# Kernel tuning notes

Measured on AMD Instinct MI355X. Metric: run time of the kernel, lower is better.

Reference implementation:

```python
import jax, jax.numpy as jnp
import numpy as np

B, T, D = 4, 1024, 1024
H, S = 16, 64            # n_heads, stalk_dim
HID = 3072               # int(D*3.0), already even
P_ADIC_BASE, P_ADIC_MAX = 2, 16


def quant6(w):
    # per-tensor symmetric 6-bit fake-quant (abs-max scale, round, clamp)
    scale = jnp.abs(w).max() / 31.0 + 1e-8
    return jnp.clip(jnp.round(w / scale), -31, 31) * scale


def q6_ste(w):
    # straight-through estimator: identity gradient
    return w + jax.lax.stop_gradient(quant6(w) - w)


def layernorm(x, g, b, eps=1e-5):
    mu = x.mean(-1, keepdims=True)
    var = ((x - mu) ** 2).mean(-1, keepdims=True)
    return (x - mu) * jax.lax.rsqrt(var + eps) * g + b


def build_p_adic_bias(t, p=P_ADIC_BASE, max_val=P_ADIC_MAX):
    idx = np.arange(t)
    d = np.abs(idx[:, None] - idx[None, :])
    nz = d > 0
    vp = np.zeros_like(d)
    work = d.copy()
    while True:
        div = nz & (work % p == 0)
        if not div.any():
            break
        vp = vp + div.astype(vp.dtype)
        work = np.where(div, work // p, work)
    vals = np.minimum(vp, max_val).astype(np.float32)
    vals = np.where(nz, vals, np.float32(max_val))
    return jnp.asarray(vals / max_val)


def setup_inputs() -> dict:
    key = jax.random.key(0)
    ks = jax.random.split(key, 12)
    sd_d = 1.0 / np.sqrt(D)
    sd_s = 1.0 / np.sqrt(S)
    sd_h = 1.0 / np.sqrt(HID)
    return {
        "x": jax.random.normal(ks[0], (B, T, D), jnp.float32),
        "wq": jax.random.normal(ks[1], (D, D), jnp.float32) * sd_d,
        "wk": jax.random.normal(ks[2], (D, D), jnp.float32) * sd_d,
        "wv": jax.random.normal(ks[3], (D, D), jnp.float32) * sd_d,
        "wo": jax.random.normal(ks[4], (D, D), jnp.float32) * sd_d,
        "su": jax.random.normal(ks[5], (S, S), jnp.float32) * sd_s,
        "sv": jax.random.normal(ks[6], (S, S), jnp.float32) * sd_s,
        "p_scale": jnp.ones((1,), jnp.float32) * 0.1,
        "norm1_g": jnp.ones((D,), jnp.float32),
        "norm1_b": jnp.zeros((D,), jnp.float32),
        "norm2_g": jnp.ones((D,), jnp.float32),
        "norm2_b": jnp.zeros((D,), jnp.float32),
        "w_up": jax.random.normal(ks[7], (HID, D), jnp.float32) * sd_d,
        "w_down": jax.random.normal(ks[8], (D, HID), jnp.float32) * sd_h,
        "theta": jnp.zeros((HID // 2,), jnp.float32),
        "mlp_norm_g": jnp.ones((HID,), jnp.float32),
        "mlp_norm_b": jnp.zeros((HID,), jnp.float32),
    }


def _sheaf_attention(xn, wq, wk, wv, wo, su, sv, p_scale):
    # projections with inline 6-bit fake-quant of weights
    Q = (xn @ q6_ste(wq).T).reshape(B, T, H, S).transpose(0, 2, 1, 3)  # [B,H,T,S]
    K = (xn @ q6_ste(wk).T).reshape(B, T, H, S).transpose(0, 2, 1, 3)
    V = (xn @ q6_ste(wv).T).reshape(B, T, H, S).transpose(0, 2, 1, 3)
    Qs = Q @ q6_ste(su).T   # stalk map on head dim
    Ks = K @ q6_ste(sv).T
    scale = 1.0 / np.sqrt(S)
    scores = jnp.einsum('bhts,bhus->bhtu', Qs, Ks) * scale
    p_bias = build_p_adic_bias(T)                     # [T,T], constant
    scores = scores + p_scale[0] * p_bias[None, None]
    causal = jnp.triu(jnp.ones((T, T), bool), k=1)
    scores = jnp.where(causal[None, None], -jnp.inf, scores)
    attn = jax.nn.softmax(scores, axis=-1)
    out = jnp.einsum('bhtu,bhus->bhts', attn, V)
    out = out.transpose(0, 2, 1, 3).reshape(B, T, D)
    return out @ q6_ste(wo).T


def _so2_mlp(xn, w_up, w_down, theta, ng, nb):
    h = xn @ q6_ste(w_up).T                          # [B,T,HID]
    hp = h.reshape(B, T, HID // 2, 2)
    a, b = hp[..., 0], hp[..., 1]
    c, s = jnp.cos(theta), jnp.sin(theta)            # [HID/2]
    rot = jnp.stack([c * a - s * b, s * a + c * b], axis=-1).reshape(B, T, HID)
    rot = layernorm(rot, ng, nb)
    rot = jax.nn.silu(rot)
    return rot @ q6_ste(w_down).T


def reference(x, wq, wk, wv, wo, su, sv, p_scale, norm1_g, norm1_b,
              norm2_g, norm2_b, w_up, w_down, theta, mlp_norm_g, mlp_norm_b):
    # pre-norm residual block: x = x + attn(ln1(x)); x = x + mlp(ln2(x))
    x = x + _sheaf_attention(layernorm(x, norm1_g, norm1_b),
                             wq, wk, wv, wo, su, sv, p_scale)
    x = x + _so2_mlp(layernorm(x, norm2_g, norm2_b),
                     w_up, w_down, theta, mlp_norm_g, mlp_norm_b)
    return x
```

## Files before the change

### kernel.cpp

```cpp
#include <hip/hip_runtime.h>
#include <stdint.h>

typedef __bf16 bf16;
typedef __attribute__((ext_vector_type(8))) __bf16 bf16x8;
typedef __attribute__((ext_vector_type(4))) __bf16 bf16x4;
typedef __attribute__((ext_vector_type(2))) __bf16 bf16x2;
typedef __attribute__((ext_vector_type(4))) float f32x4;

#define GLOBAL_AS __attribute__((address_space(1)))
#define LDS_AS __attribute__((address_space(3)))

static __device__ __forceinline__ bf16 f2bf(float f) {
  unsigned u = __builtin_bit_cast(unsigned, f);
  u += 0x7fffu + ((u >> 16) & 1u);
  unsigned short h = (unsigned short)(u >> 16);
  return __builtin_bit_cast(bf16, h);
}

static __device__ __forceinline__ float waveSum(float v) {
  #pragma unroll
  for (int o = 32; o > 0; o >>= 1) v += __shfl_xor(v, o);
  return v;
}
static __device__ __forceinline__ float waveMax(float v) {
  #pragma unroll
  for (int o = 32; o > 0; o >>= 1) v = fmaxf(v, __shfl_xor(v, o));
  return v;
}

struct QTask { const float* src; bf16* dst; int n; int slot; int blk0; };
struct QTasks { QTask t[8]; };

__global__ __launch_bounds__(256) void absmax_all(QTasks qt, unsigned* amax) {
  int ti = 0;
  #pragma unroll
  for (int i = 1; i < 8; ++i) if ((int)blockIdx.x >= qt.t[i].blk0) ti = i;
  const QTask tk = qt.t[ti];
  const int base = (blockIdx.x - tk.blk0) * 4096;
  const float4* s4 = (const float4*)(tk.src + base);
  float m = 0.f;
  #pragma unroll
  for (int i = 0; i < 4; ++i) {
    float4 w = s4[i * 256 + threadIdx.x];
    m = fmaxf(m, fmaxf(fmaxf(fabsf(w.x), fabsf(w.y)), fmaxf(fabsf(w.z), fabsf(w.w))));
  }
  m = waveMax(m);
  __shared__ float red[4];
  if ((threadIdx.x & 63) == 0) red[threadIdx.x >> 6] = m;
  __syncthreads();
  if (threadIdx.x == 0) {
    float mm = fmaxf(fmaxf(red[0], red[1]), fmaxf(red[2], red[3]));
    atomicMax(amax + tk.slot, __float_as_uint(mm));
  }
}

__global__ __launch_bounds__(256) void quant_all(QTasks qt, const unsigned* amax) {
  int ti = 0;
  #pragma unroll
  for (int i = 1; i < 8; ++i) if ((int)blockIdx.x >= qt.t[i].blk0) ti = i;
  const QTask tk = qt.t[ti];
  const float scale = __uint_as_float(amax[tk.slot]) / 31.0f + 1e-8f;
  const int base = (blockIdx.x - tk.blk0) * 4096;
  const float4* s4 = (const float4*)(tk.src + base);
  bf16x4* d4 = (bf16x4*)(tk.dst + base);
  #pragma unroll
  for (int i = 0; i < 4; ++i) {
    float4 w = s4[i * 256 + threadIdx.x];
    bf16x4 o;
    float q;
    q = fminf(31.f, fmaxf(-31.f, rintf(w.x / scale))); o[0] = f2bf(q * scale);
    q = fminf(31.f, fmaxf(-31.f, rintf(w.y / scale))); o[1] = f2bf(q * scale);
    q = fminf(31.f, fmaxf(-31.f, rintf(w.z / scale))); o[2] = f2bf(q * scale);
    q = fminf(31.f, fmaxf(-31.f, rintf(w.w / scale))); o[3] = f2bf(q * scale);
    d4[i * 256 + threadIdx.x] = o;
  }
}

__global__ __launch_bounds__(256) void ln_kernel(const float* __restrict__ x,
                                                 const float* __restrict__ g,
                                                 const float* __restrict__ b,
                                                 bf16* __restrict__ out) {
  const int row = blockIdx.x, tid = threadIdx.x;
  const float4 v = ((const float4*)(x + (size_t)row * 1024))[tid];
  float s = v.x + v.y + v.z + v.w;
  float ss = v.x * v.x + v.y * v.y + v.z * v.z + v.w * v.w;
  s = waveSum(s); ss = waveSum(ss);
  __shared__ float rs[4], rq[4];
  if ((tid & 63) == 0) { rs[tid >> 6] = s; rq[tid >> 6] = ss; }
  __syncthreads();
  s = rs[0] + rs[1] + rs[2] + rs[3];
  ss = rq[0] + rq[1] + rq[2] + rq[3];
  const float mu = s * (1.f / 1024.f);
  const float var = ss * (1.f / 1024.f) - mu * mu;
  const float rstd = rsqrtf(var + 1e-5f);
  const float4 gv = ((const float4*)g)[tid];
  const float4 bv = ((const float4*)b)[tid];
  bf16x4 o;
  o[0] = f2bf((v.x - mu) * rstd * gv.x + bv.x);
  o[1] = f2bf((v.y - mu) * rstd * gv.y + bv.y);
  o[2] = f2bf((v.z - mu) * rstd * gv.z + bv.z);
  o[3] = f2bf((v.w - mu) * rstd * gv.w + bv.w);
  ((bf16x4*)(out + (size_t)row * 1024))[tid] = o;
}

__global__ __launch_bounds__(256) void gemm_bt(const bf16* __restrict__ A,
                                               const bf16* __restrict__ B,
                                               bf16* __restrict__ C,
                                               int M, int N, int K) {
  constexpr int BM = 128, BN = 128, BK = 32;
  __shared__ bf16 As[BM * BK];
  __shared__ bf16 Bs[BN * BK];
  const int tid = threadIdx.x;
  const int wave = tid >> 6, lane = tid & 63, quad = lane >> 4, l16 = lane & 15;
  const int bm0 = blockIdx.y * BM, bn0 = blockIdx.x * BN;
  const int wr = (wave >> 1) * 64, wc = (wave & 1) * 64;
  f32x4 acc[4][4] = {};

  for (int k0 = 0; k0 < K; k0 += BK) {
    __syncthreads();
    #pragma unroll
    for (int i = 0; i < 2; ++i) {
      const int id = tid + i * 256;
      const int r = id >> 2, c = (id & 3) * 8;
      __builtin_amdgcn_global_load_lds(
          (GLOBAL_AS void*)(A + (size_t)(bm0 + r) * K + k0 + c),
          (LDS_AS void*)(As + (size_t)(i * 256 + wave * 64) * 8), 16, 0, 0);
      __builtin_amdgcn_global_load_lds(
          (GLOBAL_AS void*)(B + (size_t)(bn0 + r) * K + k0 + c),
          (LDS_AS void*)(Bs + (size_t)(i * 256 + wave * 64) * 8), 16, 0, 0);
    }
    __syncthreads();
    bf16x8 af[4], bfr[4];
    #pragma unroll
    for (int mi = 0; mi < 4; ++mi)
      af[mi] = *(const bf16x8*)(As + (wr + mi * 16 + l16) * BK + quad * 8);
    #pragma unroll
    for (int ni = 0; ni < 4; ++ni)
      bfr[ni] = *(const bf16x8*)(Bs + (wc + ni * 16 + l16) * BK + quad * 8);
    #pragma unroll
    for (int mi = 0; mi < 4; ++mi)
      #pragma unroll
      for (int ni = 0; ni < 4; ++ni)
        acc[mi][ni] = __builtin_amdgcn_mfma_f32_16x16x32_bf16(af[mi], bfr[ni], acc[mi][ni], 0, 0, 0);
  }

  #pragma unroll
  for (int mi = 0; mi < 4; ++mi)
    #pragma unroll
    for (int ni = 0; ni < 4; ++ni)
      #pragma unroll
      for (int reg = 0; reg < 4; ++reg) {
        const int row = bm0 + wr + mi * 16 + quad * 4 + reg;
        const int col = bn0 + wc + ni * 16 + l16;
        C[(size_t)row * N + col] = f2bf(acc[mi][ni][reg]);
      }
}

__global__ __launch_bounds__(256) void gemm_bt_split(const bf16* __restrict__ A,
                                                     const bf16* __restrict__ B,
                                                     float* __restrict__ P,
                                                     int M, int N, int Kfull, int Kper) {
  constexpr int BM = 128, BN = 128, BK = 32;
  __shared__ bf16 As[BM * BK];
  __shared__ bf16 Bs[BN * BK];
  const int tid = threadIdx.x;
  const int wave = tid >> 6, lane = tid & 63, quad = lane >> 4, l16 = lane & 15;
  const int bm0 = blockIdx.y * BM, bn0 = blockIdx.x * BN;
  const int wr = (wave >> 1) * 64, wc = (wave & 1) * 64;
  const int kbeg = blockIdx.z * Kper, kend = kbeg + Kper;
  float* Pz = P + (size_t)blockIdx.z * M * N;
  f32x4 acc[4][4] = {};

  for (int k0 = kbeg; k0 < kend; k0 += BK) {
    __syncthreads();
    #pragma unroll
    for (int i = 0; i < 2; ++i) {
      const int id = tid + i * 256;
      const int r = id >> 2, c = (id & 3) * 8;
      __builtin_amdgcn_global_load_lds(
          (GLOBAL_AS void*)(A + (size_t)(bm0 + r) * Kfull + k0 + c),
          (LDS_AS void*)(As + (size_t)(i * 256 + wave * 64) * 8), 16, 0, 0);
      __builtin_amdgcn_global_load_lds(
          (GLOBAL_AS void*)(B + (size_t)(bn0 + r) * Kfull + k0 + c),
          (LDS_AS void*)(Bs + (size_t)(i * 256 + wave * 64) * 8), 16, 0, 0);
    }
    __syncthreads();
    bf16x8 af[4], bfr[4];
    #pragma unroll
    for (int mi = 0; mi < 4; ++mi)
      af[mi] = *(const bf16x8*)(As + (wr + mi * 16 + l16) * BK + quad * 8);
    #pragma unroll
    for (int ni = 0; ni < 4; ++ni)
      bfr[ni] = *(const bf16x8*)(Bs + (wc + ni * 16 + l16) * BK + quad * 8);
    #pragma unroll
    for (int mi = 0; mi < 4; ++mi)
      #pragma unroll
      for (int ni = 0; ni < 4; ++ni)
        acc[mi][ni] = __builtin_amdgcn_mfma_f32_16x16x32_bf16(af[mi], bfr[ni], acc[mi][ni], 0, 0, 0);
  }

  #pragma unroll
  for (int mi = 0; mi < 4; ++mi)
    #pragma unroll
    for (int ni = 0; ni < 4; ++ni)
      #pragma unroll
      for (int reg = 0; reg < 4; ++reg) {
        const int row = bm0 + wr + mi * 16 + quad * 4 + reg;
        const int col = bn0 + wc + ni * 16 + l16;
        Pz[(size_t)row * N + col] = acc[mi][ni][reg];
      }
}

__global__ __launch_bounds__(256) void reduce_wo_ln(const float* __restrict__ x,
                                                    const float* __restrict__ P,
                                                    const float* __restrict__ g,
                                                    const float* __restrict__ b,
                                                    float* __restrict__ y,
                                                    bf16* __restrict__ lnout) {
  const int row = blockIdx.x, tid = threadIdx.x;
  const size_t base = (size_t)row * 1024;
  const float4 vx = ((const float4*)(x + base))[tid];
  const float4 p0 = ((const float4*)(P + base))[tid];
  const float4 p1 = ((const float4*)(P + base + (size_t)4096 * 1024))[tid];
  float4 v;
  v.x = vx.x + p0.x + p1.x;
  v.y = vx.y + p0.y + p1.y;
  v.z = vx.z + p0.z + p1.z;
  v.w = vx.w + p0.w + p1.w;
  ((float4*)(y + base))[tid] = v;
  float s = v.x + v.y + v.z + v.w;
  float ss = v.x * v.x + v.y * v.y + v.z * v.z + v.w * v.w;
  s = waveSum(s); ss = waveSum(ss);
  __shared__ float rs[4], rq[4];
  if ((tid & 63) == 0) { rs[tid >> 6] = s; rq[tid >> 6] = ss; }
  __syncthreads();
  s = rs[0] + rs[1] + rs[2] + rs[3];
  ss = rq[0] + rq[1] + rq[2] + rq[3];
  const float mu = s * (1.f / 1024.f);
  const float var = ss * (1.f / 1024.f) - mu * mu;
  const float rstd = rsqrtf(var + 1e-5f);
  const float4 gv = ((const float4*)g)[tid];
  const float4 bv = ((const float4*)b)[tid];
  bf16x4 o;
  o[0] = f2bf((v.x - mu) * rstd * gv.x + bv.x);
  o[1] = f2bf((v.y - mu) * rstd * gv.y + bv.y);
  o[2] = f2bf((v.z - mu) * rstd * gv.z + bv.z);
  o[3] = f2bf((v.w - mu) * rstd * gv.w + bv.w);
  ((bf16x4*)(lnout + base))[tid] = o;
}

__global__ __launch_bounds__(256) void reduce_down(float* __restrict__ y,
                                                   const float* __restrict__ P) {
  const size_t i = (size_t)blockIdx.x * 256 + threadIdx.x;
  const float4 vy = ((const float4*)y)[i];
  const float4 p0 = ((const float4*)P)[i];
  const float4 p1 = ((const float4*)(P + (size_t)4096 * 1024))[i];
  float4 v;
  v.x = vy.x + p0.x + p1.x;
  v.y = vy.y + p0.y + p1.y;
  v.z = vy.z + p0.z + p1.z;
  v.w = vy.w + p0.w + p1.w;
  ((float4*)y)[i] = v;
}

__global__ __launch_bounds__(256) void stalk_kernel(const bf16* __restrict__ QKV,
                                                    const bf16* __restrict__ Su,
                                                    const bf16* __restrict__ Sv,
                                                    bf16* __restrict__ Qsout,
                                                    bf16* __restrict__ Ksout) {
  constexpr int LDP = 72;
  const int sel = blockIdx.y;
  const bf16* W = sel ? Sv : Su;
  const bf16* src = QKV + (sel ? 1024 : 0);
  bf16* out = sel ? Ksout : Qsout;
  const int vbase = blockIdx.x * 128;
  const int tid = threadIdx.x, wave = tid >> 6, lane = tid & 63, quad = lane >> 4, l16 = lane & 15;
  __shared__ bf16 Ws[64 * LDP];
  #pragma unroll
  for (int i = 0; i < 2; ++i) {
    const int cid = tid + i * 256;
    const int n = cid >> 3, c8 = (cid & 7) * 8;
    *(bf16x8*)(Ws + n * LDP + c8) = *(const bf16x8*)(W + n * 64 + c8);
  }
  __syncthreads();
  f32x4 acc[2][4] = {};
  #pragma unroll
  for (int mi = 0; mi < 2; ++mi) {
    const int v = vbase + wave * 32 + mi * 16 + l16;
    const bf16* arow = src + (size_t)(v >> 4) * 3072 + (v & 15) * 64;
    const bf16x8 a0 = *(const bf16x8*)(arow + quad * 8);
    const bf16x8 a1 = *(const bf16x8*)(arow + 32 + quad * 8);
    #pragma unroll
    for (int ni = 0; ni < 4; ++ni) {
      const bf16x8 b0 = *(const bf16x8*)(Ws + (ni * 16 + l16) * LDP + quad * 8);
      const bf16x8 b1 = *(const bf16x8*)(Ws + (ni * 16 + l16) * LDP + 32 + quad * 8);
      acc[mi][ni] = __builtin_amdgcn_mfma_f32_16x16x32_bf16(a0, b0, acc[mi][ni], 0, 0, 0);
      acc[mi][ni] = __builtin_amdgcn_mfma_f32_16x16x32_bf16(a1, b1, acc[mi][ni], 0, 0, 0);
    }
  }
  #pragma unroll
  for (int mi = 0; mi < 2; ++mi)
    #pragma unroll
    for (int ni = 0; ni < 4; ++ni)
      #pragma unroll
      for (int reg = 0; reg < 4; ++reg) {
        const int v = vbase + wave * 32 + mi * 16 + quad * 4 + reg;
        const int b = v >> 14, t = (v >> 4) & 1023, h = v & 15;
        out[(((size_t)(b * 16 + h)) * 1024 + t) * 64 + ni * 16 + l16] = f2bf(acc[mi][ni][reg]);
      }
}

__global__ __launch_bounds__(256) void v_transpose(const bf16* __restrict__ QKV,
                                                   bf16* __restrict__ Vt) {
  constexpr int LDP = 72;
  const int bh = blockIdx.x, b = bh >> 4, h = bh & 15;
  const int t0 = blockIdx.y * 64;
  const int tid = threadIdx.x;
  __shared__ bf16 tile[64 * LDP];
  #pragma unroll
  for (int i = 0; i < 2; ++i) {
    const int cid = tid + i * 256;
    const int t = cid >> 3, c8 = (cid & 7) * 8;
    *(bf16x8*)(tile + t * LDP + c8) =
        *(const bf16x8*)(QKV + ((size_t)(b * 1024 + t0 + t)) * 3072 + 2048 + h * 64 + c8);
  }
  __syncthreads();
  #pragma unroll
  for (int i = 0; i < 2; ++i) {
    const int cid = tid + i * 256;
    const int s = cid >> 3, t8 = (cid & 7) * 8;
    bf16x8 o;
    #pragma unroll
    for (int j = 0; j < 8; ++j) o[j] = tile[(t8 + j) * LDP + s];
    *(bf16x8*)(Vt + ((size_t)(bh * 64 + s)) * 1024 + t0 + t8) = o;
  }
}

__global__ __launch_bounds__(256) void attn_flash(const bf16* __restrict__ Qs,
                                                  const bf16* __restrict__ Ks,
                                                  const bf16* __restrict__ Vtg,
                                                  const float* __restrict__ p_scale_ptr,
                                                  bf16* __restrict__ out) {
  constexpr int LDP = 72;
  const int bh = blockIdx.x;
  const int b = bh >> 4, h = bh & 15;
  const int ttile = 15 - (int)blockIdx.y;
  const int t0 = ttile * 64;
  const int tid = threadIdx.x, wave = tid >> 6, lane = tid & 63, quad = lane >> 4, l16 = lane & 15;

  __shared__ bf16 Kst[64 * LDP];
  __shared__ bf16 Vt[64 * LDP];
  __shared__ bf16 Plds[4][16 * LDP];

  const float pscale2 = p_scale_ptr[0] * 1.44269504f;
  const float sc2 = 0.125f * 1.44269504f;

  const bf16* Qb = Qs + ((size_t)bh * 1024 + t0) * 64;
  const bf16* Kb = Ks + ((size_t)bh * 1024) * 64;
  const bf16* Vb = Vtg + ((size_t)bh * 64) * 1024;

  const int trow = wave * 16 + l16;
  const bf16x8 qf0 = *(const bf16x8*)(Qb + trow * 64 + quad * 8);
  const bf16x8 qf1 = *(const bf16x8*)(Qb + trow * 64 + 32 + quad * 8);

  float m[4], lsum[4];
  f32x4 Oacc[4] = {};
  #pragma unroll
  for (int r = 0; r < 4; ++r) { m[r] = -1e30f; lsum[r] = 0.f; }

  bf16x8 st[4];
  auto loadTile = [&](int u0) {
    #pragma unroll
    for (int i = 0; i < 2; ++i) {
      const int cid = tid + i * 256;
      st[i] = *(const bf16x8*)(Kb + (size_t)u0 * 64 + cid * 8);
      st[2 + i] = *(const bf16x8*)(Vb + (size_t)(cid >> 3) * 1024 + u0 + (cid & 7) * 8);
    }
  };
  loadTile(0);

  for (int ut = 0; ut <= ttile; ++ut) {
    const int u0 = ut * 64;
    #pragma unroll
    for (int i = 0; i < 2; ++i) {
      const int cid = tid + i * 256;
      const int r = cid >> 3, c8 = (cid & 7) * 8;
      *(bf16x8*)(Kst + r * LDP + c8) = st[i];
      *(bf16x8*)(Vt + r * LDP + c8) = st[2 + i];
    }
    __syncthreads();
    if (ut < ttile) loadTile(u0 + 64);

    f32x4 sc[4];
    #pragma unroll
    for (int ni = 0; ni < 4; ++ni) {
      const bf16x8 k0 = *(const bf16x8*)(Kst + (ni * 16 + l16) * LDP + quad * 8);
      const bf16x8 k1 = *(const bf16x8*)(Kst + (ni * 16 + l16) * LDP + 32 + quad * 8);
      f32x4 z = {};
      z = __builtin_amdgcn_mfma_f32_16x16x32_bf16(qf0, k0, z, 0, 0, 0);
      z = __builtin_amdgcn_mfma_f32_16x16x32_bf16(qf1, k1, z, 0, 0, 0);
      sc[ni] = z;
    }
    const bool diag = (ut == ttile);
    float pv[4][4];
    #pragma unroll
    for (int reg = 0; reg < 4; ++reg) {
      const int t = t0 + wave * 16 + quad * 4 + reg;
      float mx = -1e30f;
      #pragma unroll
      for (int ni = 0; ni < 4; ++ni) {
        const int u = u0 + ni * 16 + l16;
        const int d = t - u;
        float v = sc[ni][reg] * sc2;
        if (diag && d < 0) {
          v = -1e30f;
        } else {
          const float bias = (d == 0) ? 1.0f : (float)__builtin_ctz(d) * 0.0625f;
          v += pscale2 * bias;
        }
        pv[reg][ni] = v;
        mx = fmaxf(mx, v);
      }
      #pragma unroll
      for (int o = 1; o < 16; o <<= 1) mx = fmaxf(mx, __shfl_xor(mx, o));
      const float mnew = fmaxf(m[reg], mx);
      const float alpha = exp2f(m[reg] - mnew);
      m[reg] = mnew;
      float rs = 0.f;
      #pragma unroll
      for (int ni = 0; ni < 4; ++ni) {
        const float p = exp2f(pv[reg][ni] - mnew);
        pv[reg][ni] = p;
        rs += p;
      }
      #pragma unroll
      for (int o = 1; o < 16; o <<= 1) rs += __shfl_xor(rs, o);
      lsum[reg] = lsum[reg] * alpha + rs;
      #pragma unroll
      for (int ni = 0; ni < 4; ++ni) Oacc[ni][reg] *= alpha;
    }
    #pragma unroll
    for (int reg = 0; reg < 4; ++reg)
      #pragma unroll
      for (int ni = 0; ni < 4; ++ni)
        Plds[wave][(quad * 4 + reg) * LDP + ni * 16 + l16] = f2bf(pv[reg][ni]);
    const bf16x8 pf0 = *(const bf16x8*)(&Plds[wave][l16 * LDP + quad * 8]);
    const bf16x8 pf1 = *(const bf16x8*)(&Plds[wave][l16 * LDP + 32 + quad * 8]);
    #pragma unroll
    for (int ni = 0; ni < 4; ++ni) {
      const bf16x8 v0 = *(const bf16x8*)(Vt + (ni * 16 + l16) * LDP + quad * 8);
      const bf16x8 v1 = *(const bf16x8*)(Vt + (ni * 16 + l16) * LDP + 32 + quad * 8);
      Oacc[ni] = __builtin_amdgcn_mfma_f32_16x16x32_bf16(pf0, v0, Oacc[ni], 0, 0, 0);
      Oacc[ni] = __builtin_amdgcn_mfma_f32_16x16x32_bf16(pf1, v1, Oacc[ni], 0, 0, 0);
    }
    __syncthreads();
  }

  #pragma unroll
  for (int ni = 0; ni < 4; ++ni)
    #pragma unroll
    for (int reg = 0; reg < 4; ++reg) {
      const int t = t0 + wave * 16 + quad * 4 + reg;
      out[((size_t)(b * 1024 + t)) * 1024 + h * 64 + ni * 16 + l16] = f2bf(Oacc[ni][reg] / lsum[reg]);
    }
}

__global__ __launch_bounds__(256) void rot_ln_silu(const bf16* __restrict__ hb,
                                                   const float* __restrict__ theta,
                                                   const float* __restrict__ g,
                                                   const float* __restrict__ bb,
                                                   bf16* __restrict__ out) {
  const int row = blockIdx.x, tid = threadIdx.x;
  const bf16* hr = hb + (size_t)row * 3072;
  float r[12];
  float s = 0.f, ss = 0.f;
  #pragma unroll
  for (int i = 0; i < 6; ++i) {
    const int p = tid + i * 256;
    const bf16x2 ab = *(const bf16x2*)(hr + 2 * p);
    const float a = (float)ab[0], b_ = (float)ab[1];
    const float th = theta[p];
    const float c = cosf(th), sn = sinf(th);
    const float r0 = c * a - sn * b_;
    const float r1 = sn * a + c * b_;
    r[2 * i] = r0; r[2 * i + 1] = r1;
    s += r0 + r1;
    ss += r0 * r0 + r1 * r1;
  }
  s = waveSum(s); ss = waveSum(ss);
  __shared__ float rs_[4], rq_[4];
  if ((tid & 63) == 0) { rs_[tid >> 6] = s; rq_[tid >> 6] = ss; }
  __syncthreads();
  s = rs_[0] + rs_[1] + rs_[2] + rs_[3];
  ss = rq_[0] + rq_[1] + rq_[2] + rq_[3];
  const float mu = s * (1.f / 3072.f);
  const float var = ss * (1.f / 3072.f) - mu * mu;
  const float rstd = rsqrtf(var + 1e-5f);
  bf16* orow = out + (size_t)row * 3072;
  #pragma unroll
  for (int i = 0; i < 6; ++i) {
    const int p = tid + i * 256;
    const float2 gv = *(const float2*)(g + 2 * p);
    const float2 bv = *(const float2*)(bb + 2 * p);
    const float y0 = (r[2 * i] - mu) * rstd * gv.x + bv.x;
    const float y1 = (r[2 * i + 1] - mu) * rstd * gv.y + bv.y;
    const float o0 = y0 / (1.f + expf(-y0));
    const float o1 = y1 / (1.f + expf(-y1));
    bf16x2 o; o[0] = f2bf(o0); o[1] = f2bf(o1);
    *(bf16x2*)(orow + 2 * p) = o;
  }
}

extern "C" void kernel_launch(void* const* d_in, const int* in_sizes, int n_in,
                              void* d_out, int out_size, void* d_ws, size_t ws_size,
                              hipStream_t stream) {
  const float* x    = (const float*)d_in[0];
  const float* wq   = (const float*)d_in[1];
  const float* wk   = (const float*)d_in[2];
  const float* wv   = (const float*)d_in[3];
  const float* wo   = (const float*)d_in[4];
  const float* su   = (const float*)d_in[5];
  const float* sv   = (const float*)d_in[6];
  const float* psc  = (const float*)d_in[7];
  const float* n1g  = (const float*)d_in[8];
  const float* n1b  = (const float*)d_in[9];
  const float* n2g  = (const float*)d_in[10];
  const float* n2b  = (const float*)d_in[11];
  const float* wup  = (const float*)d_in[12];
  const float* wdn  = (const float*)d_in[13];
  const float* th   = (const float*)d_in[14];
  const float* mg   = (const float*)d_in[15];
  const float* mb   = (const float*)d_in[16];
  float* outp = (float*)d_out;

  char* ws = (char*)d_ws;
  size_t off = 0;
  auto alloc = [&](size_t bytes) { size_t o = off; off += (bytes + 255) & ~(size_t)255; return o; };
  unsigned* amax = (unsigned*)(ws + alloc(32));
  bf16* Wqkv  = (bf16*)(ws + alloc((size_t)3072 * 1024 * 2));
  bf16* Wo    = (bf16*)(ws + alloc((size_t)1024 * 1024 * 2));
  bf16* Su    = (bf16*)(ws + alloc((size_t)64 * 64 * 2));
  bf16* Sv    = (bf16*)(ws + alloc((size_t)64 * 64 * 2));
  bf16* Wup   = (bf16*)(ws + alloc((size_t)3072 * 1024 * 2));
  bf16* Wdn   = (bf16*)(ws + alloc((size_t)1024 * 3072 * 2));
  bf16* lnbuf = (bf16*)(ws + alloc((size_t)4096 * 1024 * 2));
  bf16* QKVb  = (bf16*)(ws + alloc((size_t)4096 * 3072 * 2));
  bf16* Qsb   = (bf16*)(ws + alloc((size_t)65536 * 64 * 2));
  bf16* Ksb   = (bf16*)(ws + alloc((size_t)65536 * 64 * 2));
  bf16* Vtg   = (bf16*)(ws + alloc((size_t)64 * 64 * 1024 * 2));
  bf16* attno = (bf16*)(ws + alloc((size_t)4096 * 1024 * 2));
  float* Pbuf = (float*)(ws + alloc((size_t)2 * 4096 * 1024 * 4));
  bf16* hbuf = QKVb;
  bf16* gbuf = Qsb;

  hipMemsetAsync(amax, 0, 32, stream);

  QTasks qt;
  int blk = 0;
  auto add = [&](int i, const float* s, bf16* d, int n) {
    qt.t[i].src = s; qt.t[i].dst = d; qt.t[i].n = n; qt.t[i].slot = i; qt.t[i].blk0 = blk;
    blk += n / 4096;
  };
  add(0, wq, Wqkv, 1024 * 1024);
  add(1, wk, Wqkv + (size_t)1024 * 1024, 1024 * 1024);
  add(2, wv, Wqkv + (size_t)2048 * 1024, 1024 * 1024);
  add(3, wo, Wo, 1024 * 1024);
  add(4, su, Su, 4096);
  add(5, sv, Sv, 4096);
  add(6, wup, Wup, 3072 * 1024);
  add(7, wdn, Wdn, 3072 * 1024);

  absmax_all<<<blk, 256, 0, stream>>>(qt, amax);
  quant_all<<<blk, 256, 0, stream>>>(qt, amax);

  ln_kernel<<<4096, 256, 0, stream>>>(x, n1g, n1b, lnbuf);
  gemm_bt<<<dim3(24, 32), 256, 0, stream>>>(lnbuf, Wqkv, QKVb, 4096, 3072, 1024);
  stalk_kernel<<<dim3(512, 2), 256, 0, stream>>>(QKVb, Su, Sv, Qsb, Ksb);
  v_transpose<<<dim3(64, 16), 256, 0, stream>>>(QKVb, Vtg);
  attn_flash<<<dim3(64, 16), 256, 0, stream>>>(Qsb, Ksb, Vtg, psc, attno);
  gemm_bt_split<<<dim3(8, 32, 2), 256, 0, stream>>>(attno, Wo, Pbuf, 4096, 1024, 1024, 512);
  reduce_wo_ln<<<4096, 256, 0, stream>>>(x, Pbuf, n2g, n2b, outp, lnbuf);
  gemm_bt<<<dim3(24, 32), 256, 0, stream>>>(lnbuf, Wup, hbuf, 4096, 3072, 1024);
  rot_ln_silu<<<4096, 256, 0, stream>>>(hbuf, th, mg, mb, gbuf);
  gemm_bt_split<<<dim3(8, 32, 2), 256, 0, stream>>>(gbuf, Wdn, Pbuf, 4096, 1024, 3072, 1536);
  reduce_down<<<4096, 256, 0, stream>>>(outp, Pbuf);
}
```

Baseline: 399.8 us.

## Fold stalk maps into Q/K weights and write head-major layout from QKV GEMM

Premultiplies the quantized Wq/Wk head blocks by the stalk matrices Su/Sv in a small kernel, so the QKV GEMM directly produces stalk-transformed Q and K. A templated epilogue then scatters them into head-major buffers, which removes the separate stalk kernel and its full QKV round trip. Split-K for the output and down projections goes from 2 to 3 slices, with an XCD-aware block remap added and the reductions extended to three partials. Rounding the fused Su·W product to bf16 changes numerics slightly. The scattered epilogue writes and the larger partial buffer add memory traffic.

Measured after the change: 408.9 us. 1.02x slower.

```diff
diff --git a/kernel.cpp b/kernel.cpp
--- a/kernel.cpp
+++ b/kernel.cpp
@@ -74,6 +74,38 @@
     q = fminf(31.f, fmaxf(-31.f, rintf(w.w / scale))); o[3] = f2bf(q * scale);
     d4[i * 256 + threadIdx.x] = o;
   }
+}
+
+__global__ __launch_bounds__(256) void premul_stalk(const bf16* __restrict__ Su,
+                                                    const bf16* __restrict__ Sv,
+                                                    const bf16* __restrict__ Wqk,
+                                                    bf16* __restrict__ Wdst) {
+  const int tensor = blockIdx.x >> 4;
+  const int h = blockIdx.x & 15;
+  const int c0 = blockIdx.y * 64;
+  const bf16* S = tensor ? Sv : Su;
+  const bf16* W = Wqk + (size_t)tensor * 1024 * 1024 + (size_t)h * 64 * 1024;
+  bf16* D = Wdst + (size_t)tensor * 1024 * 1024 + (size_t)h * 64 * 1024;
+  const int tid = threadIdx.x;
+  const int i = tid >> 2;
+  const int c = c0 + (tid & 3) * 16;
+  bf16x8 srow[8];
+  #pragma unroll
+  for (int k = 0; k < 8; ++k) srow[k] = *(const bf16x8*)(S + i * 64 + k * 8);
+  float acc[16] = {};
+  #pragma unroll
+  for (int j = 0; j < 64; ++j) {
+    const float s = (float)srow[j >> 3][j & 7];
+    const bf16x8 w0 = *(const bf16x8*)(W + (size_t)j * 1024 + c);
+    const bf16x8 w1 = *(const bf16x8*)(W + (size_t)j * 1024 + c + 8);
+    #pragma unroll
+    for (int k = 0; k < 8; ++k) { acc[k] += s * (float)w0[k]; acc[8 + k] += s * (float)w1[k]; }
+  }
+  bf16x8 o0, o1;
+  #pragma unroll
+  for (int k = 0; k < 8; ++k) { o0[k] = f2bf(acc[k]); o1[k] = f2bf(acc[8 + k]); }
+  *(bf16x8*)(D + (size_t)i * 1024 + c) = o0;
+  *(bf16x8*)(D + (size_t)i * 1024 + c + 8) = o1;
 }
 
 __global__ __launch_bounds__(256) void ln_kernel(const float* __restrict__ x,
@@ -103,9 +135,13 @@
   ((bf16x4*)(out + (size_t)row * 1024))[tid] = o;
 }
 
+template <int EPI>
 __global__ __launch_bounds__(256) void gemm_bt(const bf16* __restrict__ A,
                                                const bf16* __restrict__ B,
                                                bf16* __restrict__ C,
+                                               bf16* __restrict__ Qsb,
+                                               bf16* __restrict__ Ksb,
+                                               bf16* __restrict__ Vbuf,
                                                int M, int N, int K) {
   constexpr int BM = 128, BN = 128, BK = 32;
   __shared__ bf16 As[BM * BK];
@@ -152,7 +188,21 @@
       for (int reg = 0; reg < 4; ++reg) {
         const int row = bm0 + wr + mi * 16 + quad * 4 + reg;
         const int col = bn0 + wc + ni * 16 + l16;
-        C[(size_t)row * N + col] = f2bf(acc[mi][ni][reg]);
+        const bf16 v = f2bf(acc[mi][ni][reg]);
+        if constexpr (EPI == 0) {
+          C[(size_t)row * N + col] = v;
+        } else {
+          const int b = row >> 10, t = row & 1023;
+          if (col < 1024) {
+            const int h = col >> 6, s = col & 63;
+            Qsb[(((size_t)(b * 16 + h)) * 1024 + t) * 64 + s] = v;
+          } else if (col < 2048) {
+            const int h = (col >> 6) & 15, s = col & 63;
+            Ksb[(((size_t)(b * 16 + h)) * 1024 + t) * 64 + s] = v;
+          } else {
+            Vbuf[(size_t)row * 1024 + (col - 2048)] = v;
+          }
+        }
       }
 }
 
@@ -165,9 +215,13 @@
   __shared__ bf16 Bs[BN * BK];
   const int tid = threadIdx.x;
   const int wave = tid >> 6, lane = tid & 63, quad = lane >> 4, l16 = lane & 15;
-  const int bm0 = blockIdx.y * BM, bn0 = blockIdx.x * BN;
+  const int lin = blockIdx.x + 8 * blockIdx.y;
+  const int xcd = lin & 7, idx = lin >> 3;
+  const int bm0 = (xcd * 4 + (idx & 3)) * BM;
+  const int bn0 = (idx >> 2) * BN;
   const int wr = (wave >> 1) * 64, wc = (wave & 1) * 64;
-  const int kbeg = blockIdx.z * Kper, kend = kbeg + Kper;
+  const int kbeg = blockIdx.z * Kper;
+  const int kend = min(kbeg + Kper, Kfull);
   float* Pz = P + (size_t)blockIdx.z * M * N;
   f32x4 acc[4][4] = {};
 
@@ -217,16 +271,18 @@
                                                     const float* __restrict__ b,
                                                     float* __restrict__ y,
                                                     bf16* __restrict__ lnout) {
+  constexpr size_t MN = (size_t)4096 * 1024;
   const int row = blockIdx.x, tid = threadIdx.x;
   const size_t base = (size_t)row * 1024;
   const float4 vx = ((const float4*)(x + base))[tid];
   const float4 p0 = ((const float4*)(P + base))[tid];
-  const float4 p1 = ((const float4*)(P + base + (size_t)4096 * 1024))[tid];
+  const float4 p1 = ((const float4*)(P + base + MN))[tid];
+  const float4 p2 = ((const float4*)(P + base + 2 * MN))[tid];
   float4 v;
-  v.x = vx.x + p0.x + p1.x;
-  v.y = vx.y + p0.y + p1.y;
-  v.z = vx.z + p0.z + p1.z;
-  v.w = vx.w + p0.w + p1.w;
+  v.x = vx.x + p0.x + p1.x + p2.x;
+  v.y = vx.y + p0.y + p1.y + p2.y;
+  v.z = vx.z + p0.z + p1.z + p2.z;
+  v.w = vx.w + p0.w + p1.w + p2.w;
   ((float4*)(y + base))[tid] = v;
   float s = v.x + v.y + v.z + v.w;
   float ss = v.x * v.x + v.y * v.y + v.z * v.z + v.w * v.w;
@@ -251,66 +307,21 @@
 
 __global__ __launch_bounds__(256) void reduce_down(float* __restrict__ y,
                                                    const float* __restrict__ P) {
+  constexpr size_t MN = (size_t)4096 * 1024;
   const size_t i = (size_t)blockIdx.x * 256 + threadIdx.x;
   const float4 vy = ((const float4*)y)[i];
   const float4 p0 = ((const float4*)P)[i];
-  const float4 p1 = ((const float4*)(P + (size_t)4096 * 1024))[i];
+  const float4 p1 = ((const float4*)(P + MN))[i];
+  const float4 p2 = ((const float4*)(P + 2 * MN))[i];
   float4 v;
-  v.x = vy.x + p0.x + p1.x;
-  v.y = vy.y + p0.y + p1.y;
-  v.z = vy.z + p0.z + p1.z;
-  v.w = vy.w + p0.w + p1.w;
+  v.x = vy.x + p0.x + p1.x + p2.x;
+  v.y = vy.y + p0.y + p1.y + p2.y;
+  v.z = vy.z + p0.z + p1.z + p2.z;
+  v.w = vy.w + p0.w + p1.w + p2.w;
   ((float4*)y)[i] = v;
 }
 
-__global__ __launch_bounds__(256) void stalk_kernel(const bf16* __restrict__ QKV,
-                                                    const bf16* __restrict__ Su,
-                                                    const bf16* __restrict__ Sv,
-                                                    bf16* __restrict__ Qsout,
-                                                    bf16* __restrict__ Ksout) {
-  constexpr int LDP = 72;
-  const int sel = blockIdx.y;
-  const bf16* W = sel ? Sv : Su;
-  const bf16* src = QKV + (sel ? 1024 : 0);
-  bf16* out = sel ? Ksout : Qsout;
-  const int vbase = blockIdx.x * 128;
-  const int tid = threadIdx.x, wave = tid >> 6, lane = tid & 63, quad = lane >> 4, l16 = lane & 15;
-  __shared__ bf16 Ws[64 * LDP];
-  #pragma unroll
-  for (int i = 0; i < 2; ++i) {
-    const int cid = tid + i * 256;
-    const int n = cid >> 3, c8 = (cid & 7) * 8;
-    *(bf16x8*)(Ws + n * LDP + c8) = *(const bf16x8*)(W + n * 64 + c8);
-  }
-  __syncthreads();
-  f32x4 acc[2][4] = {};
-  #pragma unroll
-  for (int mi = 0; mi < 2; ++mi) {
-    const int v = vbase + wave * 32 + mi * 16 + l16;
-    const bf16* arow = src + (size_t)(v >> 4) * 3072 + (v & 15) * 64;
-    const bf16x8 a0 = *(const bf16x8*)(arow + quad * 8);
-    const bf16x8 a1 = *(const bf16x8*)(arow + 32 + quad * 8);
-    #pragma unroll
-    for (int ni = 0; ni < 4; ++ni) {
-      const bf16x8 b0 = *(const bf16x8*)(Ws + (ni * 16 + l16) * LDP + quad * 8);
-      const bf16x8 b1 = *(const bf16x8*)(Ws + (ni * 16 + l16) * LDP + 32 + quad * 8);
-      acc[mi][ni] = __builtin_amdgcn_mfma_f32_16x16x32_bf16(a0, b0, acc[mi][ni], 0, 0, 0);
-      acc[mi][ni] = __builtin_amdgcn_mfma_f32_16x16x32_bf16(a1, b1, acc[mi][ni], 0, 0, 0);
-    }
-  }
-  #pragma unroll
-  for (int mi = 0; mi < 2; ++mi)
-    #pragma unroll
-    for (int ni = 0; ni < 4; ++ni)
-      #pragma unroll
-      for (int reg = 0; reg < 4; ++reg) {
-        const int v = vbase + wave * 32 + mi * 16 + quad * 4 + reg;
-        const int b = v >> 14, t = (v >> 4) & 1023, h = v & 15;
-        out[(((size_t)(b * 16 + h)) * 1024 + t) * 64 + ni * 16 + l16] = f2bf(acc[mi][ni][reg]);
-      }
-}
-
-__global__ __launch_bounds__(256) void v_transpose(const bf16* __restrict__ QKV,
+__global__ __launch_bounds__(256) void v_transpose(const bf16* __restrict__ Vbuf,
                                                    bf16* __restrict__ Vt) {
   constexpr int LDP = 72;
   const int bh = blockIdx.x, b = bh >> 4, h = bh & 15;
@@ -322,7 +333,7 @@
     const int cid = tid + i * 256;
     const int t = cid >> 3, c8 = (cid & 7) * 8;
     *(bf16x8*)(tile + t * LDP + c8) =
-        *(const bf16x8*)(QKV + ((size_t)(b * 1024 + t0 + t)) * 3072 + 2048 + h * 64 + c8);
+        *(const bf16x8*)(Vbuf + ((size_t)(b * 1024 + t0 + t)) * 1024 + h * 64 + c8);
   }
   __syncthreads();
   #pragma unroll
@@ -536,22 +547,25 @@
   char* ws = (char*)d_ws;
   size_t off = 0;
   auto alloc = [&](size_t bytes) { size_t o = off; off += (bytes + 255) & ~(size_t)255; return o; };
+  constexpr size_t MB84 = (size_t)4096 * 1024 * 2;
   unsigned* amax = (unsigned*)(ws + alloc(32));
-  bf16* Wqkv  = (bf16*)(ws + alloc((size_t)3072 * 1024 * 2));
+  bf16* Su    = (bf16*)(ws + alloc(4096 * 2));
+  bf16* Sv    = (bf16*)(ws + alloc(4096 * 2));
   bf16* Wo    = (bf16*)(ws + alloc((size_t)1024 * 1024 * 2));
-  bf16* Su    = (bf16*)(ws + alloc((size_t)64 * 64 * 2));
-  bf16* Sv    = (bf16*)(ws + alloc((size_t)64 * 64 * 2));
   bf16* Wup   = (bf16*)(ws + alloc((size_t)3072 * 1024 * 2));
   bf16* Wdn   = (bf16*)(ws + alloc((size_t)1024 * 3072 * 2));
-  bf16* lnbuf = (bf16*)(ws + alloc((size_t)4096 * 1024 * 2));
-  bf16* QKVb  = (bf16*)(ws + alloc((size_t)4096 * 3072 * 2));
-  bf16* Qsb   = (bf16*)(ws + alloc((size_t)65536 * 64 * 2));
-  bf16* Ksb   = (bf16*)(ws + alloc((size_t)65536 * 64 * 2));
-  bf16* Vtg   = (bf16*)(ws + alloc((size_t)64 * 64 * 1024 * 2));
-  bf16* attno = (bf16*)(ws + alloc((size_t)4096 * 1024 * 2));
-  float* Pbuf = (float*)(ws + alloc((size_t)2 * 4096 * 1024 * 4));
-  bf16* hbuf = QKVb;
-  bf16* gbuf = Qsb;
+  bf16* Wqkv2 = (bf16*)(ws + alloc((size_t)3072 * 1024 * 2));
+  bf16* Wqk   = (bf16*)(ws + alloc((size_t)2048 * 1024 * 2));
+  bf16* lnbuf = (bf16*)(ws + alloc(MB84));
+  char* arena = ws + alloc(6 * MB84);
+  bf16* Qsb   = (bf16*)(arena);
+  bf16* Ksb   = (bf16*)(arena + MB84);
+  bf16* Vtg   = (bf16*)(arena + 2 * MB84);
+  bf16* Vbuf  = (bf16*)(arena + 3 * MB84);
+  bf16* attno = (bf16*)(arena + 4 * MB84);
+  bf16* hbuf  = (bf16*)(arena);
+  bf16* gbuf  = (bf16*)(arena + 3 * MB84);
+  float* Pbuf = (float*)(ws + alloc((size_t)3 * 4096 * 1024 * 4));
 
   hipMemsetAsync(amax, 0, 32, stream);
 
@@ -561,9 +575,9 @@
     qt.t[i].src = s; qt.t[i].dst = d; qt.t[i].n = n; qt.t[i].slot = i; qt.t[i].blk0 = blk;
     blk += n / 4096;
   };
-  add(0, wq, Wqkv, 1024 * 1024);
-  add(1, wk, Wqkv + (size_t)1024 * 1024, 1024 * 1024);
-  add(2, wv, Wqkv + (size_t)2048 * 1024, 1024 * 1024);
+  add(0, wq, Wqk, 1024 * 1024);
+  add(1, wk, Wqk + (size_t)1024 * 1024, 1024 * 1024);
+  add(2, wv, Wqkv2 + (size_t)2048 * 1024, 1024 * 1024);
   add(3, wo, Wo, 1024 * 1024);
   add(4, su, Su, 4096);
   add(5, sv, Sv, 4096);
@@ -572,16 +586,16 @@
 
   absmax_all<<<blk, 256, 0, stream>>>(qt, amax);
   quant_all<<<blk, 256, 0, stream>>>(qt, amax);
+  premul_stalk<<<dim3(32, 16), 256, 0, stream>>>(Su, Sv, Wqk, Wqkv2);
 
   ln_kernel<<<4096, 256, 0, stream>>>(x, n1g, n1b, lnbuf);
-  gemm_bt<<<dim3(24, 32), 256, 0, stream>>>(lnbuf, Wqkv, QKVb, 4096, 3072, 1024);
-  stalk_kernel<<<dim3(512, 2), 256, 0, stream>>>(QKVb, Su, Sv, Qsb, Ksb);
-  v_transpose<<<dim3(64, 16), 256, 0, stream>>>(QKVb, Vtg);
+  gemm_bt<1><<<dim3(24, 32), 256, 0, stream>>>(lnbuf, Wqkv2, nullptr, Qsb, Ksb, Vbuf, 4096, 3072, 1024);
+  v_transpose<<<dim3(64, 16), 256, 0, stream>>>(Vbuf, Vtg);
   attn_flash<<<dim3(64, 16), 256, 0, stream>>>(Qsb, Ksb, Vtg, psc, attno);
-  gemm_bt_split<<<dim3(8, 32, 2), 256, 0, stream>>>(attno, Wo, Pbuf, 4096, 1024, 1024, 512);
+  gemm_bt_split<<<dim3(8, 32, 3), 256, 0, stream>>>(attno, Wo, Pbuf, 4096, 1024, 1024, 352);
   reduce_wo_ln<<<4096, 256, 0, stream>>>(x, Pbuf, n2g, n2b, outp, lnbuf);
-  gemm_bt<<<dim3(24, 32), 256, 0, stream>>>(lnbuf, Wup, hbuf, 4096, 3072, 1024);
+  gemm_bt<0><<<dim3(24, 32), 256, 0, stream>>>(lnbuf, Wup, hbuf, nullptr, nullptr, nullptr, 4096, 3072, 1024);
   rot_ln_silu<<<4096, 256, 0, stream>>>(hbuf, th, mg, mb, gbuf);
-  gemm_bt_split<<<dim3(8, 32, 2), 256, 0, stream>>>(gbuf, Wdn, Pbuf, 4096, 1024, 3072, 1536);
+  gemm_bt_split<<<dim3(8, 32, 3), 256, 0, stream>>>(gbuf, Wdn, Pbuf, 4096, 1024, 3072, 1024);
   reduce_down<<<4096, 256, 0, stream>>>(outp, Pbuf);
 }
```
